# Performance work log

Measured on AMD Instinct MI355X. Metric: run time of the kernel, lower is better.

Reference implementation:

```python
import jax, jax.numpy as jnp
import numpy as np

EPS = 1e-8

def _cosine_sim_matrix(a, b):
    # Faithful to sim_func: full N x N cosine similarity via normalized matmul
    an = a / jnp.maximum(jnp.linalg.norm(a, axis=-1, keepdims=True), EPS)
    bn = b / jnp.maximum(jnp.linalg.norm(b, axis=-1, keepdims=True), EPS)
    return jnp.einsum('nd,md->nm', an, bn)  # [N, N]

def setup_inputs() -> dict:
    key = jax.random.key(0)
    k1, k2 = jax.random.split(key)
    N, D = 8192, 512
    x = jax.random.normal(k1, (N, D), dtype=jnp.float32)
    x_target = jax.random.normal(k2, (N, D), dtype=jnp.float32)
    return {"x": x, "x_target": x_target}

def reference(x, x_target):
    sim = _cosine_sim_matrix(x, x_target)          # [N, N]
    diag = jnp.diagonal(sim)                        # [N]
    loss = 2.0 - 2.0 * jnp.mean(diag)
    return loss
```

## Files before the change

kernel.cpp:

```cpp
#include <hip/hip_runtime.h>

#define NROWS 8192
#define DIM   512
#define EPS   1e-8f

__global__ __launch_bounds__(1024) void byol_fused(const float* __restrict__ x,
                                                   const float* __restrict__ t,
                                                   float* __restrict__ out) {
    const int wave = threadIdx.x >> 6;
    const int lane = threadIdx.x & 63;
    const int row0 = blockIdx.x * 32 + wave * 2;

    float acc = 0.f;
#pragma unroll
    for (int r = 0; r < 2; ++r) {
        const int row = row0 + r;
        const float4* __restrict__ xr = (const float4*)(x + (size_t)row * DIM);
        const float4* __restrict__ tr = (const float4*)(t + (size_t)row * DIM);

        float dot = 0.f, nx = 0.f, nt = 0.f;
#pragma unroll
        for (int j = 0; j < 2; ++j) {
            float4 a = xr[j * 64 + lane];
            float4 b = tr[j * 64 + lane];
            dot += a.x * b.x + a.y * b.y + a.z * b.z + a.w * b.w;
            nx  += a.x * a.x + a.y * a.y + a.z * a.z + a.w * a.w;
            nt  += b.x * b.x + b.y * b.y + b.z * b.z + b.w * b.w;
        }

#pragma unroll
        for (int off = 32; off > 0; off >>= 1) {
            dot += __shfl_xor(dot, off, 64);
            nx  += __shfl_xor(nx,  off, 64);
            nt  += __shfl_xor(nt,  off, 64);
        }
        acc += dot / (fmaxf(sqrtf(nx), EPS) * fmaxf(sqrtf(nt), EPS));
    }

    __shared__ float s[16];
    if (lane == 0) s[wave] = acc;
    __syncthreads();
    if (threadIdx.x == 0) {
        float p = 0.f;
#pragma unroll
        for (int i = 0; i < 16; ++i) p += s[i];
        atomicAdd(out, (2.0f / 256.0f) - p * (1.0f / 4096.0f));
    }
}

extern "C" void kernel_launch(void* const* d_in, const int* in_sizes, int n_in,
                              void* d_out, int out_size, void* d_ws, size_t ws_size,
                              hipStream_t stream) {
    const float* x = (const float*)d_in[0];
    const float* t = (const float*)d_in[1];
    float* out     = (float*)d_out;

    byol_fused<<<256, 1024, 0, stream>>>(x, t, out);
}
```

Before: 75.61 us.

## Split into per-row partial kernel plus single-block reduce, drop atomics

Replaces the single fused kernel (256 blocks of 1024 threads, two rows per wave, atomicAdd into the output) with two kernels. The first runs 2048 blocks of 256 threads, one row per wave, loading with nontemporal loads and writing a per-block partial to workspace. A second one-block kernel reduces the partials and writes the loss directly. This removes the atomics and the reliance on a pre-zeroed output and spreads the work over more, smaller blocks, at the cost of an extra kernel launch and a workspace round trip.

```diff
diff --git a/kernel.cpp b/kernel.cpp
--- a/kernel.cpp
+++ b/kernel.cpp
@@ -3,48 +3,62 @@
 #define NROWS 8192
 #define DIM   512
 #define EPS   1e-8f
+#define NBLK1 2048
 
-__global__ __launch_bounds__(1024) void byol_fused(const float* __restrict__ x,
-                                                   const float* __restrict__ t,
-                                                   float* __restrict__ out) {
+typedef float floatx4 __attribute__((ext_vector_type(4)));
+
+__global__ __launch_bounds__(256) void byol_rows(const float* __restrict__ x,
+                                                 const float* __restrict__ t,
+                                                 float* __restrict__ partial) {
     const int wave = threadIdx.x >> 6;
     const int lane = threadIdx.x & 63;
-    const int row0 = blockIdx.x * 32 + wave * 2;
+    const int row  = blockIdx.x * 4 + wave;
 
-    float acc = 0.f;
-#pragma unroll
-    for (int r = 0; r < 2; ++r) {
-        const int row = row0 + r;
-        const float4* __restrict__ xr = (const float4*)(x + (size_t)row * DIM);
-        const float4* __restrict__ tr = (const float4*)(t + (size_t)row * DIM);
+    const floatx4* __restrict__ xr = (const floatx4*)(x + (size_t)row * DIM);
+    const floatx4* __restrict__ tr = (const floatx4*)(t + (size_t)row * DIM);
 
-        float dot = 0.f, nx = 0.f, nt = 0.f;
-#pragma unroll
-        for (int j = 0; j < 2; ++j) {
-            float4 a = xr[j * 64 + lane];
-            float4 b = tr[j * 64 + lane];
-            dot += a.x * b.x + a.y * b.y + a.z * b.z + a.w * b.w;
-            nx  += a.x * a.x + a.y * a.y + a.z * a.z + a.w * a.w;
-            nt  += b.x * b.x + b.y * b.y + b.z * b.z + b.w * b.w;
-        }
+    const floatx4 a0 = __builtin_nontemporal_load(&xr[lane]);
+    const floatx4 a1 = __builtin_nontemporal_load(&xr[64 + lane]);
+    const floatx4 b0 = __builtin_nontemporal_load(&tr[lane]);
+    const floatx4 b1 = __builtin_nontemporal_load(&tr[64 + lane]);
+
+    float dot = a0.x * b0.x + a0.y * b0.y + a0.z * b0.z + a0.w * b0.w
+              + a1.x * b1.x + a1.y * b1.y + a1.z * b1.z + a1.w * b1.w;
+    float nx  = a0.x * a0.x + a0.y * a0.y + a0.z * a0.z + a0.w * a0.w
+              + a1.x * a1.x + a1.y * a1.y + a1.z * a1.z + a1.w * a1.w;
+    float nt  = b0.x * b0.x + b0.y * b0.y + b0.z * b0.z + b0.w * b0.w
+              + b1.x * b1.x + b1.y * b1.y + b1.z * b1.z + b1.w * b1.w;
 
 #pragma unroll
-        for (int off = 32; off > 0; off >>= 1) {
-            dot += __shfl_xor(dot, off, 64);
-            nx  += __shfl_xor(nx,  off, 64);
-            nt  += __shfl_xor(nt,  off, 64);
-        }
-        acc += dot / (fmaxf(sqrtf(nx), EPS) * fmaxf(sqrtf(nt), EPS));
+    for (int off = 32; off > 0; off >>= 1) {
+        dot += __shfl_xor(dot, off, 64);
+        nx  += __shfl_xor(nx,  off, 64);
+        nt  += __shfl_xor(nt,  off, 64);
     }
+    const float cosv = dot / (fmaxf(sqrtf(nx), EPS) * fmaxf(sqrtf(nt), EPS));
+
+    __shared__ float s[4];
+    if (lane == 0) s[wave] = cosv;
+    __syncthreads();
+    if (threadIdx.x == 0)
+        partial[blockIdx.x] = s[0] + s[1] + s[2] + s[3];
+}
+
+__global__ __launch_bounds__(1024) void byol_reduce(const float* __restrict__ partial,
+                                                    float* __restrict__ out) {
+    float v = partial[threadIdx.x] + partial[threadIdx.x + 1024];
+#pragma unroll
+    for (int off = 32; off > 0; off >>= 1)
+        v += __shfl_xor(v, off, 64);
 
     __shared__ float s[16];
-    if (lane == 0) s[wave] = acc;
+    if ((threadIdx.x & 63) == 0) s[threadIdx.x >> 6] = v;
     __syncthreads();
     if (threadIdx.x == 0) {
         float p = 0.f;
 #pragma unroll
         for (int i = 0; i < 16; ++i) p += s[i];
-        atomicAdd(out, (2.0f / 256.0f) - p * (1.0f / 4096.0f));
+        out[0] = 2.0f - p * (1.0f / 4096.0f);
     }
 }
 
@@ -53,7 +67,9 @@
                               hipStream_t stream) {
     const float* x = (const float*)d_in[0];
     const float* t = (const float*)d_in[1];
+    float* ws      = (float*)d_ws;
     float* out     = (float*)d_out;
 
-    byol_fused<<<256, 1024, 0, stream>>>(x, t, out);
+    byol_rows<<<NBLK1, 256, 0, stream>>>(x, t, ws);
+    byol_reduce<<<1, 1024, 0, stream>>>(ws, out);
 }
```

Measured after the change: 78.55 us. 3.9% more time.
